# Performance work log

Measured on AMD Instinct MI355X. Metric: run time of the kernel, lower is better.

## Reference

```python
import jax, jax.numpy as jnp
import numpy as np

CHUNK = 1024  # rows per tile; keeps the (CHUNK, out, in) broadcast tensor at ~64 MB


def _minplus_2d(x2d, a):
    # x2d: (N, in), a: (out, in) -> (N, out); y[n, o] = min_i x[n, i] + a[o, i]
    n, din = x2d.shape
    xc = x2d.reshape(n // CHUNK, CHUNK, din)

    def tile(xb):
        # (CHUNK, 1, in) + (out, in) -> min over in -> (CHUNK, out)
        return jnp.min(xb[:, None, :] + a[None, :, :], axis=-1)

    return jax.lax.map(tile, xc).reshape(n, -1)


def setup_inputs() -> dict:
    key = jax.random.key(0)
    k1, k2, k3 = jax.random.split(key, 3)
    x = jax.random.normal(k1, (16, 2048, 128), dtype=jnp.float32)
    weight = jax.random.normal(k2, (128, 128), dtype=jnp.float32)
    bias = jax.random.normal(k3, (128,), dtype=jnp.float32)
    return {"x": x, "weight": weight, "bias": bias}


def reference(x, weight, bias):
    prefix = x.shape[:-1]
    y = _minplus_2d(x.reshape(-1, x.shape[-1]), weight) + bias  # min-plus semiring matmul + bias
    return y.reshape(*prefix, weight.shape[0])
```

## Files before the change

### kernel.cpp

```cpp
#include <hip/hip_runtime.h>
#include <hip/hip_bf16.h>
#include <math.h>


typedef __fp16 h2 __attribute__((ext_vector_type(2)));
typedef __fp16 h4 __attribute__((ext_vector_type(4)));
typedef __fp16 h8 __attribute__((ext_vector_type(8)));

constexpr int K     = 128;
constexpr int BM    = 128;
constexpr int BN    = 64;
constexpr int LDRH2 = 68;

__global__ __launch_bounds__(256, 2)
void minplus_kernel(const float* __restrict__ x,
                    const float* __restrict__ w,
                    const float* __restrict__ bias,
                    float* __restrict__ out)
{
    __shared__ h2 lds[(BM + BN) * LDRH2];
    h2* xs = lds;
    h2* ws = lds + BM * LDRH2;

    const int tid = threadIdx.x;
    const int rt  = blockIdx.x & 255;
    const int ct  = blockIdx.x >> 8;

    const float* xsrc = x + (size_t)rt * BM * K;
    const float* wsrc = w + (size_t)ct * BN * K;

    #pragma unroll
    for (int p = 0; p < 16; ++p) {
        int c   = p * 256 + tid;
        int row = c >> 5;
        int q   = c & 31;
        float4 v = *(const float4*)(xsrc + row * K + q * 4);
        h2 a = __builtin_amdgcn_cvt_pkrtz(v.x, v.y);
        h2 b = __builtin_amdgcn_cvt_pkrtz(v.z, v.w);
        *(h4*)(xs + row * LDRH2 + q * 2) = __builtin_shufflevector(a, b, 0, 1, 2, 3);
    }
    #pragma unroll
    for (int p = 0; p < 8; ++p) {
        int c   = p * 256 + tid;
        int row = c >> 5;
        int q   = c & 31;
        float4 v = *(const float4*)(wsrc + row * K + q * 4);
        h2 a = __builtin_amdgcn_cvt_pkrtz(v.x, v.y);
        h2 b = __builtin_amdgcn_cvt_pkrtz(v.z, v.w);
        *(h4*)(ws + row * LDRH2 + q * 2) = __builtin_shufflevector(a, b, 0, 1, 2, 3);
    }
    __syncthreads();

    const int ty = tid >> 4;
    const int tx = tid & 15;
    const h2* xbp = xs + ty * LDRH2;
    const h2* wbp = ws + tx * LDRH2;

    h2 hbig;
    hbig.x = (__fp16)65504.0f;
    hbig.y = (__fp16)65504.0f;
    h2 acc[8][4];
    #pragma unroll
    for (int m = 0; m < 8; ++m)
        #pragma unroll
        for (int n = 0; n < 4; ++n)
            acc[m][n] = hbig;

    #pragma unroll 4
    for (int kc = 0; kc < 16; ++kc) {
        h8 xv0 = *(const h8*)(xbp + 0 * 16 * LDRH2 + kc * 4);
        h8 xv1 = *(const h8*)(xbp + 1 * 16 * LDRH2 + kc * 4);
        h8 xv2 = *(const h8*)(xbp + 2 * 16 * LDRH2 + kc * 4);
        h8 xv3 = *(const h8*)(xbp + 3 * 16 * LDRH2 + kc * 4);
        h8 xv4 = *(const h8*)(xbp + 4 * 16 * LDRH2 + kc * 4);
        h8 xv5 = *(const h8*)(xbp + 5 * 16 * LDRH2 + kc * 4);
        h8 xv6 = *(const h8*)(xbp + 6 * 16 * LDRH2 + kc * 4);
        h8 xv7 = *(const h8*)(xbp + 7 * 16 * LDRH2 + kc * 4);
        h8 wv0 = *(const h8*)(wbp + 0 * 16 * LDRH2 + kc * 4);
        h8 wv1 = *(const h8*)(wbp + 1 * 16 * LDRH2 + kc * 4);
        h8 wv2 = *(const h8*)(wbp + 2 * 16 * LDRH2 + kc * 4);
        h8 wv3 = *(const h8*)(wbp + 3 * 16 * LDRH2 + kc * 4);

#define UPD(m, n, XV, WV)                                                     \
        {                                                                     \
            h8 t  = XV + WV;                             \
            h2 t0 = __builtin_shufflevector(t, t, 0, 1);                      \
            h2 t1 = __builtin_shufflevector(t, t, 2, 3);                      \
            h2 t2 = __builtin_shufflevector(t, t, 4, 5);                      \
            h2 t3 = __builtin_shufflevector(t, t, 6, 7);                      \
            h2 u  = __builtin_elementwise_min(t0, t1);                        \
            h2 v  = __builtin_elementwise_min(t2, t3);                        \
            h2 uv = __builtin_elementwise_min(u, v);                          \
            acc[m][n] = __builtin_elementwise_min(acc[m][n], uv);             \
        }
        UPD(0, 0, xv0, wv0) UPD(0, 1, xv0, wv1) UPD(0, 2, xv0, wv2) UPD(0, 3, xv0, wv3)
        UPD(1, 0, xv1, wv0) UPD(1, 1, xv1, wv1) UPD(1, 2, xv1, wv2) UPD(1, 3, xv1, wv3)
        UPD(2, 0, xv2, wv0) UPD(2, 1, xv2, wv1) UPD(2, 2, xv2, wv2) UPD(2, 3, xv2, wv3)
        UPD(3, 0, xv3, wv0) UPD(3, 1, xv3, wv1) UPD(3, 2, xv3, wv2) UPD(3, 3, xv3, wv3)
        UPD(4, 0, xv4, wv0) UPD(4, 1, xv4, wv1) UPD(4, 2, xv4, wv2) UPD(4, 3, xv4, wv3)
        UPD(5, 0, xv5, wv0) UPD(5, 1, xv5, wv1) UPD(5, 2, xv5, wv2) UPD(5, 3, xv5, wv3)
        UPD(6, 0, xv6, wv0) UPD(6, 1, xv6, wv1) UPD(6, 2, xv6, wv2) UPD(6, 3, xv6, wv3)
        UPD(7, 0, xv7, wv0) UPD(7, 1, xv7, wv1) UPD(7, 2, xv7, wv2) UPD(7, 3, xv7, wv3)
#undef UPD
    }

    const int rowbase = rt * BM + ty;
    const int colbase = ct * BN + tx;
    #pragma unroll
    for (int n = 0; n < 4; ++n) {
        float b = bias[colbase + 16 * n];
        #pragma unroll
        for (int m = 0; m < 8; ++m) {
            h2 a = acc[m][n];
            out[(size_t)(rowbase + 16 * m) * 128 + colbase + 16 * n] =
                fminf((float)a.x, (float)a.y) + b;
        }
    }
}

extern "C" void kernel_launch(void* const* d_in, const int* in_sizes, int n_in,
                              void* d_out, int out_size, void* d_ws, size_t ws_size,
                              hipStream_t stream) {
    const float* x    = (const float*)d_in[0];
    const float* w    = (const float*)d_in[1];
    const float* bias = (const float*)d_in[2];
    float* out = (float*)d_out;

    int nrows  = in_sizes[0] / K;
    int blocks = (nrows / BM) * (K / BN);
    minplus_kernel<<<blocks, 256, 0, stream>>>(x, w, bias, out);
}
```

Measured before the change: 28.65 us.

## Pre-convert weights to fp16 and read them from global/L1 instead of LDS

Adds a small kernel that converts the weight matrix to fp16 in the workspace once per call. The main kernel now gives each block 64 rows and all 128 output columns, staging only x in LDS and reading weight vectors directly from global memory, which should mostly hit cache. Each block no longer converts fp32 weights into LDS, and x is no longer loaded twice (once per column tile). The cost is a second kernel launch, a wider per-thread weight load set, and weight reads that no longer come from LDS.

```diff
diff --git a/kernel.cpp b/kernel.cpp
--- a/kernel.cpp
+++ b/kernel.cpp
@@ -8,29 +8,30 @@
 typedef __fp16 h8 __attribute__((ext_vector_type(8)));
 
 constexpr int K     = 128;
-constexpr int BM    = 128;
-constexpr int BN    = 64;
+constexpr int BM    = 64;
 constexpr int LDRH2 = 68;
+
+__global__ void cvt_w_kernel(const float* __restrict__ w, __fp16* __restrict__ wh) {
+    int i = blockIdx.x * 256 + threadIdx.x;
+    float4 v = *(const float4*)(w + (size_t)i * 4);
+    h2 a = __builtin_amdgcn_cvt_pkrtz(v.x, v.y);
+    h2 b = __builtin_amdgcn_cvt_pkrtz(v.z, v.w);
+    *(h4*)(wh + (size_t)i * 4) = __builtin_shufflevector(a, b, 0, 1, 2, 3);
+}
 
 __global__ __launch_bounds__(256, 2)
 void minplus_kernel(const float* __restrict__ x,
-                    const float* __restrict__ w,
+                    const __fp16* __restrict__ wh,
                     const float* __restrict__ bias,
                     float* __restrict__ out)
 {
-    __shared__ h2 lds[(BM + BN) * LDRH2];
-    h2* xs = lds;
-    h2* ws = lds + BM * LDRH2;
+    __shared__ h2 xs[BM * LDRH2];
 
     const int tid = threadIdx.x;
-    const int rt  = blockIdx.x & 255;
-    const int ct  = blockIdx.x >> 8;
-
-    const float* xsrc = x + (size_t)rt * BM * K;
-    const float* wsrc = w + (size_t)ct * BN * K;
+    const float* xsrc = x + (size_t)blockIdx.x * BM * K;
 
     #pragma unroll
-    for (int p = 0; p < 16; ++p) {
+    for (int p = 0; p < 8; ++p) {
         int c   = p * 256 + tid;
         int row = c >> 5;
         int q   = c & 31;
@@ -39,47 +40,45 @@
         h2 b = __builtin_amdgcn_cvt_pkrtz(v.z, v.w);
         *(h4*)(xs + row * LDRH2 + q * 2) = __builtin_shufflevector(a, b, 0, 1, 2, 3);
     }
-    #pragma unroll
-    for (int p = 0; p < 8; ++p) {
-        int c   = p * 256 + tid;
-        int row = c >> 5;
-        int q   = c & 31;
-        float4 v = *(const float4*)(wsrc + row * K + q * 4);
-        h2 a = __builtin_amdgcn_cvt_pkrtz(v.x, v.y);
-        h2 b = __builtin_amdgcn_cvt_pkrtz(v.z, v.w);
-        *(h4*)(ws + row * LDRH2 + q * 2) = __builtin_shufflevector(a, b, 0, 1, 2, 3);
-    }
     __syncthreads();
 
     const int ty = tid >> 4;
     const int tx = tid & 15;
     const h2* xbp = xs + ty * LDRH2;
-    const h2* wbp = ws + tx * LDRH2;
+
+    const __fp16* wp0 = wh + (size_t)(tx +   0) * K;
+    const __fp16* wp1 = wh + (size_t)(tx +  16) * K;
+    const __fp16* wp2 = wh + (size_t)(tx +  32) * K;
+    const __fp16* wp3 = wh + (size_t)(tx +  48) * K;
+    const __fp16* wp4 = wh + (size_t)(tx +  64) * K;
+    const __fp16* wp5 = wh + (size_t)(tx +  80) * K;
+    const __fp16* wp6 = wh + (size_t)(tx +  96) * K;
+    const __fp16* wp7 = wh + (size_t)(tx + 112) * K;
 
     h2 hbig;
     hbig.x = (__fp16)65504.0f;
     hbig.y = (__fp16)65504.0f;
-    h2 acc[8][4];
+    h2 acc[4][8];
     #pragma unroll
-    for (int m = 0; m < 8; ++m)
+    for (int m = 0; m < 4; ++m)
         #pragma unroll
-        for (int n = 0; n < 4; ++n)
+        for (int n = 0; n < 8; ++n)
             acc[m][n] = hbig;
 
-    #pragma unroll 4
+    #pragma unroll 2
     for (int kc = 0; kc < 16; ++kc) {
         h8 xv0 = *(const h8*)(xbp + 0 * 16 * LDRH2 + kc * 4);
         h8 xv1 = *(const h8*)(xbp + 1 * 16 * LDRH2 + kc * 4);
         h8 xv2 = *(const h8*)(xbp + 2 * 16 * LDRH2 + kc * 4);
         h8 xv3 = *(const h8*)(xbp + 3 * 16 * LDRH2 + kc * 4);
-        h8 xv4 = *(const h8*)(xbp + 4 * 16 * LDRH2 + kc * 4);
-        h8 xv5 = *(const h8*)(xbp + 5 * 16 * LDRH2 + kc * 4);
-        h8 xv6 = *(const h8*)(xbp + 6 * 16 * LDRH2 + kc * 4);
-        h8 xv7 = *(const h8*)(xbp + 7 * 16 * LDRH2 + kc * 4);
-        h8 wv0 = *(const h8*)(wbp + 0 * 16 * LDRH2 + kc * 4);
-        h8 wv1 = *(const h8*)(wbp + 1 * 16 * LDRH2 + kc * 4);
-        h8 wv2 = *(const h8*)(wbp + 2 * 16 * LDRH2 + kc * 4);
-        h8 wv3 = *(const h8*)(wbp + 3 * 16 * LDRH2 + kc * 4);
+        h8 wv0 = *(const h8*)(wp0 + kc * 8);
+        h8 wv1 = *(const h8*)(wp1 + kc * 8);
+        h8 wv2 = *(const h8*)(wp2 + kc * 8);
+        h8 wv3 = *(const h8*)(wp3 + kc * 8);
+        h8 wv4 = *(const h8*)(wp4 + kc * 8);
+        h8 wv5 = *(const h8*)(wp5 + kc * 8);
+        h8 wv6 = *(const h8*)(wp6 + kc * 8);
+        h8 wv7 = *(const h8*)(wp7 + kc * 8);
 
 #define UPD(m, n, XV, WV)                                                     \
         {                                                                     \
@@ -93,26 +92,23 @@
             h2 uv = __builtin_elementwise_min(u, v);                          \
             acc[m][n] = __builtin_elementwise_min(acc[m][n], uv);             \
         }
-        UPD(0, 0, xv0, wv0) UPD(0, 1, xv0, wv1) UPD(0, 2, xv0, wv2) UPD(0, 3, xv0, wv3)
-        UPD(1, 0, xv1, wv0) UPD(1, 1, xv1, wv1) UPD(1, 2, xv1, wv2) UPD(1, 3, xv1, wv3)
-        UPD(2, 0, xv2, wv0) UPD(2, 1, xv2, wv1) UPD(2, 2, xv2, wv2) UPD(2, 3, xv2, wv3)
-        UPD(3, 0, xv3, wv0) UPD(3, 1, xv3, wv1) UPD(3, 2, xv3, wv2) UPD(3, 3, xv3, wv3)
-        UPD(4, 0, xv4, wv0) UPD(4, 1, xv4, wv1) UPD(4, 2, xv4, wv2) UPD(4, 3, xv4, wv3)
-        UPD(5, 0, xv5, wv0) UPD(5, 1, xv5, wv1) UPD(5, 2, xv5, wv2) UPD(5, 3, xv5, wv3)
-        UPD(6, 0, xv6, wv0) UPD(6, 1, xv6, wv1) UPD(6, 2, xv6, wv2) UPD(6, 3, xv6, wv3)
-        UPD(7, 0, xv7, wv0) UPD(7, 1, xv7, wv1) UPD(7, 2, xv7, wv2) UPD(7, 3, xv7, wv3)
+#define ROW(m, XV)                                                            \
+        UPD(m, 0, XV, wv0) UPD(m, 1, XV, wv1) UPD(m, 2, XV, wv2)              \
+        UPD(m, 3, XV, wv3) UPD(m, 4, XV, wv4) UPD(m, 5, XV, wv5)              \
+        UPD(m, 6, XV, wv6) UPD(m, 7, XV, wv7)
+        ROW(0, xv0) ROW(1, xv1) ROW(2, xv2) ROW(3, xv3)
+#undef ROW
 #undef UPD
     }
 
-    const int rowbase = rt * BM + ty;
-    const int colbase = ct * BN + tx;
+    const int rowbase = blockIdx.x * BM + ty;
     #pragma unroll
-    for (int n = 0; n < 4; ++n) {
-        float b = bias[colbase + 16 * n];
+    for (int n = 0; n < 8; ++n) {
+        float b = bias[tx + 16 * n];
         #pragma unroll
-        for (int m = 0; m < 8; ++m) {
+        for (int m = 0; m < 4; ++m) {
             h2 a = acc[m][n];
-            out[(size_t)(rowbase + 16 * m) * 128 + colbase + 16 * n] =
+            out[(size_t)(rowbase + 16 * m) * 128 + tx + 16 * n] =
                 fminf((float)a.x, (float)a.y) + b;
         }
     }
@@ -125,8 +121,11 @@
     const float* w    = (const float*)d_in[1];
     const float* bias = (const float*)d_in[2];
     float* out = (float*)d_out;
+    __fp16* wh = (__fp16*)d_ws;
+
+    cvt_w_kernel<<<16, 256, 0, stream>>>(w, wh);
 
     int nrows  = in_sizes[0] / K;
-    int blocks = (nrows / BM) * (K / BN);
-    minplus_kernel<<<blocks, 256, 0, stream>>>(x, w, bias, out);
+    int blocks = nrows / BM;
+    minplus_kernel<<<blocks, 256, 0, stream>>>(x, wh, bias, out);
 }
```

New measurement: 43.26 us. 1.51x slower.

## Cover all output columns per block and use XOR-swizzled LDS layout

Applied to the files above, without the earlier changes.

Each block now computes a 128-row by full 128-column output tile with 512 threads, instead of splitting the columns across two blocks. This halves the number of x loads and fp16 conversions. Padded LDS rows are replaced with an unpadded 256-byte row layout using an XOR swizzle to avoid bank conflicts. The costs are 64 KB of LDS per block, which limits occupancy, and half as many blocks (256), which may underfill the GPU's compute units.

```diff
diff --git a/kernel.cpp b/kernel.cpp
--- a/kernel.cpp
+++ b/kernel.cpp
@@ -7,54 +7,50 @@
 typedef __fp16 h4 __attribute__((ext_vector_type(4)));
 typedef __fp16 h8 __attribute__((ext_vector_type(8)));
 
-constexpr int K     = 128;
-constexpr int BM    = 128;
-constexpr int BN    = 64;
-constexpr int LDRH2 = 68;
+constexpr int K  = 128;
+constexpr int BM = 128;
 
-__global__ __launch_bounds__(256, 2)
+__global__ __launch_bounds__(512, 2)
 void minplus_kernel(const float* __restrict__ x,
                     const float* __restrict__ w,
                     const float* __restrict__ bias,
                     float* __restrict__ out)
 {
-    __shared__ h2 lds[(BM + BN) * LDRH2];
-    h2* xs = lds;
-    h2* ws = lds + BM * LDRH2;
+    __shared__ char lds[65536];
 
     const int tid = threadIdx.x;
-    const int rt  = blockIdx.x & 255;
-    const int ct  = blockIdx.x >> 8;
-
-    const float* xsrc = x + (size_t)rt * BM * K;
-    const float* wsrc = w + (size_t)ct * BN * K;
+    const float* xsrc = x + (size_t)blockIdx.x * BM * K;
 
     #pragma unroll
-    for (int p = 0; p < 16; ++p) {
-        int c   = p * 256 + tid;
+    for (int p = 0; p < 8; ++p) {
+        int c   = p * 512 + tid;
         int row = c >> 5;
         int q   = c & 31;
         float4 v = *(const float4*)(xsrc + row * K + q * 4);
         h2 a = __builtin_amdgcn_cvt_pkrtz(v.x, v.y);
         h2 b = __builtin_amdgcn_cvt_pkrtz(v.z, v.w);
-        *(h4*)(xs + row * LDRH2 + q * 2) = __builtin_shufflevector(a, b, 0, 1, 2, 3);
+        int byte = row * 256 + ((q * 8) ^ ((row & 7) << 4));
+        *(h4*)(lds + byte) = __builtin_shufflevector(a, b, 0, 1, 2, 3);
     }
     #pragma unroll
     for (int p = 0; p < 8; ++p) {
-        int c   = p * 256 + tid;
+        int c   = p * 512 + tid;
         int row = c >> 5;
         int q   = c & 31;
-        float4 v = *(const float4*)(wsrc + row * K + q * 4);
+        float4 v = *(const float4*)(w + row * K + q * 4);
         h2 a = __builtin_amdgcn_cvt_pkrtz(v.x, v.y);
         h2 b = __builtin_amdgcn_cvt_pkrtz(v.z, v.w);
-        *(h4*)(ws + row * LDRH2 + q * 2) = __builtin_shufflevector(a, b, 0, 1, 2, 3);
+        int byte = 32768 + row * 256 + ((q * 8) ^ ((row & 7) << 4));
+        *(h4*)(lds + byte) = __builtin_shufflevector(a, b, 0, 1, 2, 3);
     }
     __syncthreads();
 
-    const int ty = tid >> 4;
-    const int tx = tid & 15;
-    const h2* xbp = xs + ty * LDRH2;
-    const h2* wbp = ws + tx * LDRH2;
+    const int ty  = tid >> 5;
+    const int tx  = tid & 31;
+    const int swx = (ty & 7) << 4;
+    const int sww = (tx & 7) << 4;
+    const char* xb = lds + ty * 256;
+    const char* wb = lds + 32768 + tx * 256;
 
     h2 hbig;
     hbig.x = (__fp16)65504.0f;
@@ -66,20 +62,22 @@
         for (int n = 0; n < 4; ++n)
             acc[m][n] = hbig;
 
-    #pragma unroll 4
+    #pragma unroll 2
     for (int kc = 0; kc < 16; ++kc) {
-        h8 xv0 = *(const h8*)(xbp + 0 * 16 * LDRH2 + kc * 4);
-        h8 xv1 = *(const h8*)(xbp + 1 * 16 * LDRH2 + kc * 4);
-        h8 xv2 = *(const h8*)(xbp + 2 * 16 * LDRH2 + kc * 4);
-        h8 xv3 = *(const h8*)(xbp + 3 * 16 * LDRH2 + kc * 4);
-        h8 xv4 = *(const h8*)(xbp + 4 * 16 * LDRH2 + kc * 4);
-        h8 xv5 = *(const h8*)(xbp + 5 * 16 * LDRH2 + kc * 4);
-        h8 xv6 = *(const h8*)(xbp + 6 * 16 * LDRH2 + kc * 4);
-        h8 xv7 = *(const h8*)(xbp + 7 * 16 * LDRH2 + kc * 4);
-        h8 wv0 = *(const h8*)(wbp + 0 * 16 * LDRH2 + kc * 4);
-        h8 wv1 = *(const h8*)(wbp + 1 * 16 * LDRH2 + kc * 4);
-        h8 wv2 = *(const h8*)(wbp + 2 * 16 * LDRH2 + kc * 4);
-        h8 wv3 = *(const h8*)(wbp + 3 * 16 * LDRH2 + kc * 4);
+        const char* xr = xb + ((kc * 16) ^ swx);
+        const char* wr = wb + ((kc * 16) ^ sww);
+        h8 xv0 = *(const h8*)(xr + 0 * 4096);
+        h8 xv1 = *(const h8*)(xr + 1 * 4096);
+        h8 xv2 = *(const h8*)(xr + 2 * 4096);
+        h8 xv3 = *(const h8*)(xr + 3 * 4096);
+        h8 xv4 = *(const h8*)(xr + 4 * 4096);
+        h8 xv5 = *(const h8*)(xr + 5 * 4096);
+        h8 xv6 = *(const h8*)(xr + 6 * 4096);
+        h8 xv7 = *(const h8*)(xr + 7 * 4096);
+        h8 wv0 = *(const h8*)(wr + 0 * 8192);
+        h8 wv1 = *(const h8*)(wr + 1 * 8192);
+        h8 wv2 = *(const h8*)(wr + 2 * 8192);
+        h8 wv3 = *(const h8*)(wr + 3 * 8192);
 
 #define UPD(m, n, XV, WV)                                                     \
         {                                                                     \
@@ -93,26 +91,22 @@
             h2 uv = __builtin_elementwise_min(u, v);                          \
             acc[m][n] = __builtin_elementwise_min(acc[m][n], uv);             \
         }
-        UPD(0, 0, xv0, wv0) UPD(0, 1, xv0, wv1) UPD(0, 2, xv0, wv2) UPD(0, 3, xv0, wv3)
-        UPD(1, 0, xv1, wv0) UPD(1, 1, xv1, wv1) UPD(1, 2, xv1, wv2) UPD(1, 3, xv1, wv3)
-        UPD(2, 0, xv2, wv0) UPD(2, 1, xv2, wv1) UPD(2, 2, xv2, wv2) UPD(2, 3, xv2, wv3)
-        UPD(3, 0, xv3, wv0) UPD(3, 1, xv3, wv1) UPD(3, 2, xv3, wv2) UPD(3, 3, xv3, wv3)
-        UPD(4, 0, xv4, wv0) UPD(4, 1, xv4, wv1) UPD(4, 2, xv4, wv2) UPD(4, 3, xv4, wv3)
-        UPD(5, 0, xv5, wv0) UPD(5, 1, xv5, wv1) UPD(5, 2, xv5, wv2) UPD(5, 3, xv5, wv3)
-        UPD(6, 0, xv6, wv0) UPD(6, 1, xv6, wv1) UPD(6, 2, xv6, wv2) UPD(6, 3, xv6, wv3)
-        UPD(7, 0, xv7, wv0) UPD(7, 1, xv7, wv1) UPD(7, 2, xv7, wv2) UPD(7, 3, xv7, wv3)
+#define ROW(m, XV)                                                            \
+        UPD(m, 0, XV, wv0) UPD(m, 1, XV, wv1) UPD(m, 2, XV, wv2) UPD(m, 3, XV, wv3)
+        ROW(0, xv0) ROW(1, xv1) ROW(2, xv2) ROW(3, xv3)
+        ROW(4, xv4) ROW(5, xv5) ROW(6, xv6) ROW(7, xv7)
+#undef ROW
 #undef UPD
     }
 
-    const int rowbase = rt * BM + ty;
-    const int colbase = ct * BN + tx;
+    const int rowbase = blockIdx.x * BM + ty;
     #pragma unroll
     for (int n = 0; n < 4; ++n) {
-        float b = bias[colbase + 16 * n];
+        float b = bias[tx + 32 * n];
         #pragma unroll
         for (int m = 0; m < 8; ++m) {
             h2 a = acc[m][n];
-            out[(size_t)(rowbase + 16 * m) * 128 + colbase + 16 * n] =
+            out[(size_t)(rowbase + 16 * m) * 128 + tx + 32 * n] =
                 fminf((float)a.x, (float)a.y) + b;
         }
     }
@@ -127,6 +121,6 @@
     float* out = (float*)d_out;
 
     int nrows  = in_sizes[0] / K;
-    int blocks = (nrows / BM) * (K / BN);
-    minplus_kernel<<<blocks, 256, 0, stream>>>(x, w, bias, out);
+    int blocks = nrows / BM;
+    minplus_kernel<<<blocks, 512, 0, stream>>>(x, w, bias, out);
 }
```

Result: no change. 28.59 us (-0.2%).
